# Kernel optimization log

Hardware: AMD Instinct MI355X
Metric: run time of the kernel (lower is better)

## Reference

```python
import jax, jax.numpy as jnp
import numpy as np

B, N, M, D = 32, 500, 500, 256
SQRT_D = 16.0
LOGIT_CLIP = 10.0


def setup_inputs() -> dict:
    key = jax.random.key(0)
    ks = jax.random.split(key, 12)
    s = 1.0 / np.sqrt(D)
    return {
        "encoded_q0": jax.random.normal(ks[0], (B, N, D), jnp.float32),
        "encoded_jobs": jax.random.normal(ks[1], (B, M, D), jnp.float32),
        "encoded_q1": jax.random.normal(ks[2], (B, N, D), jnp.float32),
        "cur_cost_mat": jax.random.uniform(ks[3], (B, N, M), jnp.float32),
        "log_scale": jnp.ones((1,), jnp.float32),
        "ninf_mask": jnp.zeros((B, N, M), jnp.float32),
        "Wq0": jax.random.normal(ks[4], (D, D), jnp.float32) * s,
        "Wq1": jax.random.normal(ks[5], (D, D), jnp.float32) * s,
        "Wk": jax.random.normal(ks[6], (D, D), jnp.float32) * s,
        "Wv": jax.random.normal(ks[7], (D, D), jnp.float32) * s,
        "alpha1": jnp.ones((1,), jnp.float32),
        "alpha2": jnp.ones((1,), jnp.float32),
    }


def reference(encoded_q0, encoded_jobs, encoded_q1, cur_cost_mat, log_scale,
              ninf_mask, Wq0, Wq1, Wk, Wv, alpha1, alpha2):
    # precomputed state (set_kv / set_q1): Linear without bias -> x @ W.T
    k = jnp.einsum('bmd,ed->bme', encoded_jobs, Wk)
    v = jnp.einsum('bmd,ed->bme', encoded_jobs, Wv)
    q1 = jnp.einsum('bnd,ed->bne', encoded_q1, Wq1)
    q0 = jnp.einsum('bnd,ed->bne', encoded_q0, Wq0)
    q = q1 + q0

    # AAFM: adaptation bias = -alpha1 * log_scale * cost (+ ninf_mask)
    exp_bias = jnp.exp(-alpha1 * log_scale * cur_cost_mat + ninf_mask)  # (B,N,M)
    exp_k = jnp.exp(k)                                                   # (B,M,D)
    num = jnp.einsum('bnm,bmd->bnd', exp_bias, exp_k * v)
    den = jnp.einsum('bnm,bmd->bnd', exp_bias, exp_k)
    weighted = jnp.nan_to_num(num / den)
    aafm_out = jax.nn.sigmoid(q) * weighted                              # (B,N,D)

    # single-head scoring against raw encoded_jobs
    score = jnp.einsum('bnd,bmd->bnm', aafm_out, encoded_jobs)
    score = score / SQRT_D - alpha2 * log_scale * cur_cost_mat
    score = LOGIT_CLIP * jnp.tanh(score) + ninf_mask
    return jax.nn.softmax(score, axis=-1)
```

## Files before the change

### kernel.cpp

```cpp
#include <hip/hip_runtime.h>
#include <math.h>

using u16 = unsigned short;
typedef __attribute__((ext_vector_type(8))) short short8;
typedef __attribute__((ext_vector_type(16))) float floatx16;

constexpr int Bc = 32, Nn = 500, Mm = 500, Dd = 256;
constexpr float LOGIT_CLIP = 10.0f;
constexpr float INV_SQRT_D = 1.0f / 16.0f;

__device__ __forceinline__ floatx16 mfma32(short8 a, short8 b, floatx16 c) {
    return __builtin_amdgcn_mfma_f32_32x32x16_bf16(a, b, c, 0, 0, 0);
}

__device__ __forceinline__ floatx16 zero16() {
    floatx16 v = {0.f,0.f,0.f,0.f,0.f,0.f,0.f,0.f,0.f,0.f,0.f,0.f,0.f,0.f,0.f,0.f};
    return v;
}

__device__ __forceinline__ void gl_lds16(const u16* g, u16* l) {
    __builtin_amdgcn_global_load_lds(
        (const __attribute__((address_space(1))) unsigned int*)g,
        (__attribute__((address_space(3))) unsigned int*)l, 16, 0, 0);
}

__device__ __forceinline__ void split1(float x, u16& h, u16& l) {
    unsigned u = __float_as_uint(x);
    unsigned rh = (u + 0x7FFFu + ((u >> 16) & 1u)) & 0xFFFF0000u;
    float fh = __uint_as_float(rh);
    float fl = x - fh;
    unsigned ul = __float_as_uint(fl);
    unsigned rl = ul + 0x7FFFu + ((ul >> 16) & 1u);
    h = (u16)(rh >> 16);
    l = (u16)(rl >> 16);
}

__device__ __forceinline__ u16 bf16rtn(float x) {
    unsigned u = __float_as_uint(x);
    return (u16)((u + 0x7FFFu + ((u >> 16) & 1u)) >> 16);
}

__device__ __forceinline__ float fast_tanh(float x) {
    return 1.0f - 2.0f / (__expf(2.0f * x) + 1.0f);
}

__device__ __forceinline__ void split8(const float4& a, const float4& c,
                                       short8& hv, short8& lv) {
    u16 hh, ll;
    split1(a.x, hh, ll); hv[0] = (short)hh; lv[0] = (short)ll;
    split1(a.y, hh, ll); hv[1] = (short)hh; lv[1] = (short)ll;
    split1(a.z, hh, ll); hv[2] = (short)hh; lv[2] = (short)ll;
    split1(a.w, hh, ll); hv[3] = (short)hh; lv[3] = (short)ll;
    split1(c.x, hh, ll); hv[4] = (short)hh; lv[4] = (short)ll;
    split1(c.y, hh, ll); hv[5] = (short)hh; lv[5] = (short)ll;
    split1(c.z, hh, ll); hv[6] = (short)hh; lv[6] = (short)ll;
    split1(c.w, hh, ll); hv[7] = (short)hh; lv[7] = (short)ll;
}


__global__ __launch_bounds__(256) void k0w_pk(const float* __restrict__ s0,
                                              const float* __restrict__ s1,
                                              const float* __restrict__ s2,
                                              const float* __restrict__ s3,
                                              u16* __restrict__ pkw) {
    const float* s = blockIdx.y == 0 ? s0 : blockIdx.y == 1 ? s1 :
                     blockIdx.y == 2 ? s2 : s3;
    const int w = blockIdx.y;
    const int flat = (blockIdx.x * 256 + threadIdx.x) * 8;
    const int i = flat >> 8, j0 = flat & 255;
    float4 a = *(const float4*)&s[flat];
    float4 c = *(const float4*)&s[flat + 4];
    short8 hv, lv;
    split8(a, c, hv, lv);
    const int dt = i >> 5, i31 = i & 31, dc = j0 >> 4, hp = (j0 >> 3) & 1;
    const size_t off = (size_t)(w * 8 + dt) * 16384 + (size_t)dc * 1024
                     + (size_t)((hp << 5) | i31) * 8;
    *(short8*)&pkw[off] = hv;
    *(short8*)&pkw[off + 512] = lv;
}

__global__ __launch_bounds__(256) void k0pk3(const float* __restrict__ s0,
                                             const float* __restrict__ s1,
                                             const float* __restrict__ s2,
                                             u16* __restrict__ d0,
                                             u16* __restrict__ d1,
                                             u16* __restrict__ d2) {
    const float* s = blockIdx.y == 0 ? s0 : blockIdx.y == 1 ? s1 : s2;
    u16* d = blockIdx.y == 0 ? d0 : blockIdx.y == 1 ? d1 : d2;
    const int bx = blockIdx.x;
    const int b = bx >> 6;
    const int chunk = bx & 63;
    const int flat = threadIdx.x * 8;
    const int lr = flat >> 8;
    const int j0 = flat & 255;
    const int pr = chunk * 8 + lr;
    short8 hv = {0,0,0,0,0,0,0,0}, lv = {0,0,0,0,0,0,0,0};
    if (pr < Nn) {
        const size_t o = ((size_t)b * Nn + pr) * Dd + j0;
        float4 a = *(const float4*)&s[o];
        float4 c = *(const float4*)&s[o + 4];
        split8(a, c, hv, lv);
    }
    const int mt = pr >> 5, r31 = pr & 31;
    const int dc = j0 >> 4, hp = (j0 >> 3) & 1;
    const size_t off = (size_t)(b * 16 + mt) * 16384 + (size_t)dc * 1024
                     + (size_t)((hp << 5) | r31) * 8;
    *(short8*)&d[off] = hv;
    *(short8*)&d[off + 512] = lv;
}

__global__ __launch_bounds__(256) void kexp_pk(const float* __restrict__ cost,
                                               const float* __restrict__ mask,
                                               const float* __restrict__ alpha1,
                                               const float* __restrict__ lsc,
                                               u16* __restrict__ pka) {
    __shared__ u16 tile[32][520];
    const float a1ls = alpha1[0] * lsc[0];
    const int b = blockIdx.x >> 4, nt = blockIdx.x & 15;
    const int t = threadIdx.x;
#pragma unroll
    for (int q = 0; q < 8; ++q) {
        const int flat = (q << 11) + (t << 3);
        const int nl = flat >> 9, m = flat & 511;
        const int n = min(nt * 32 + nl, Nn - 1);
        const size_t o = ((size_t)b * Nn + n) * Mm + m;
        ushort4 w0 = {0, 0, 0, 0}, w1 = {0, 0, 0, 0};
        if (m <= 488) {
            float4 c0 = *(const float4*)&cost[o];
            float4 c1 = *(const float4*)&cost[o + 4];
            float4 k0 = *(const float4*)&mask[o];
            float4 k1 = *(const float4*)&mask[o + 4];
            w0.x = bf16rtn(__expf(fmaf(-a1ls, c0.x, k0.x)));
            w0.y = bf16rtn(__expf(fmaf(-a1ls, c0.y, k0.y)));
            w0.z = bf16rtn(__expf(fmaf(-a1ls, c0.z, k0.z)));
            w0.w = bf16rtn(__expf(fmaf(-a1ls, c0.w, k0.w)));
            w1.x = bf16rtn(__expf(fmaf(-a1ls, c1.x, k1.x)));
            w1.y = bf16rtn(__expf(fmaf(-a1ls, c1.y, k1.y)));
            w1.z = bf16rtn(__expf(fmaf(-a1ls, c1.z, k1.z)));
            w1.w = bf16rtn(__expf(fmaf(-a1ls, c1.w, k1.w)));
        } else if (m == 496) {
            float4 c0 = *(const float4*)&cost[o];
            float4 k0 = *(const float4*)&mask[o];
            w0.x = bf16rtn(__expf(fmaf(-a1ls, c0.x, k0.x)));
            w0.y = bf16rtn(__expf(fmaf(-a1ls, c0.y, k0.y)));
            w0.z = bf16rtn(__expf(fmaf(-a1ls, c0.z, k0.z)));
            w0.w = bf16rtn(__expf(fmaf(-a1ls, c0.w, k0.w)));
        }
        *(ushort4*)&tile[nl][m] = w0;
        *(ushort4*)&tile[nl][m + 4] = w1;
    }
    __syncthreads();
    const int lane = t & 63, wvv = t >> 6;
    const int n31 = lane & 31, hh = lane >> 5;
    const size_t pbase = (size_t)(b * 16 + nt) * 16384 + (size_t)lane * 8;
#pragma unroll
    for (int q = 0; q < 8; ++q) {
        const int mc = wvv * 8 + q;
        short8 v = *(const short8*)&tile[n31][mc * 16 + hh * 8];
        *(short8*)&pka[pbase + (size_t)mc * 512] = v;
    }
}

__global__ __launch_bounds__(256) void k1_kv(const u16* __restrict__ pkj,
                                             const u16* __restrict__ pkw,
                                             u16* __restrict__ pkb) {
    const int lane = threadIdx.x & 63, wv = threadIdx.x >> 6;
    const int l31 = lane & 31, h = lane >> 5;
    const int b = blockIdx.z;
    const int dt = blockIdx.y * 4 + wv;
    const int mt = blockIdx.x;
    const int M0 = mt * 32;

    const size_t wk  = (size_t)dt * 16384 + (size_t)lane * 8;
    const size_t wvb = (size_t)(8 + dt) * 16384 + (size_t)lane * 8;
    const size_t jb  = (size_t)(b * 16 + mt) * 16384 + (size_t)lane * 8;

    floatx16 ak = zero16(), av = zero16();

    short8 buf[3][6];
#define K1L(S, DC) { \
    buf[S][0] = *(const short8*)(pkw + wk  + (size_t)(DC) * 1024); \
    buf[S][1] = *(const short8*)(pkw + wk  + (size_t)(DC) * 1024 + 512); \
    buf[S][2] = *(const short8*)(pkw + wvb + (size_t)(DC) * 1024); \
    buf[S][3] = *(const short8*)(pkw + wvb + (size_t)(DC) * 1024 + 512); \
    buf[S][4] = *(const short8*)(pkj + jb  + (size_t)(DC) * 1024); \
    buf[S][5] = *(const short8*)(pkj + jb  + (size_t)(DC) * 1024 + 512); }

    K1L(0, 0)
    K1L(1, 1)
#pragma unroll
    for (int it = 0; it < 16; ++it) {
        if (it + 2 < 16) { K1L((it + 2) % 3, it + 2) }
        const int c = it % 3;
        ak = mfma32(buf[c][0], buf[c][4], ak);
        ak = mfma32(buf[c][0], buf[c][5], ak);
        ak = mfma32(buf[c][1], buf[c][4], ak);
        av = mfma32(buf[c][2], buf[c][4], av);
        av = mfma32(buf[c][2], buf[c][5], av);
        av = mfma32(buf[c][3], buf[c][4], av);
    }
#undef K1L

    const int hp = (l31 >> 3) & 1, ee = l31 & 7, mcl = l31 >> 4;
    const size_t sb0 = ((size_t)b * 8 + dt) * 65536
                     + (size_t)(mt * 2 + mcl) * 2048 + (size_t)hp * 256 + ee;
    const bool v0 = (M0 + l31) < Mm;
#pragma unroll
    for (int r = 0; r < 16; ++r) {
        const int d31 = (r & 3) + ((r >> 2) << 3) + (h << 2);
        const size_t o = sb0 + (size_t)d31 * 8;
        u16 hh, ll;
        const float ek = v0 ? __expf(ak[r]) : 0.f;
        const float ev = v0 ? ek * av[r] : 0.f;
        split1(ek, hh, ll); pkb[o] = hh; pkb[o + 512] = ll;
        split1(ev, hh, ll); pkb[o + 1024] = hh; pkb[o + 1536] = ll;
    }
}

__global__ __launch_bounds__(256) void k2_q(const u16* __restrict__ pkq0,
                                            const u16* __restrict__ pkq1,
                                            const u16* __restrict__ pkw,
                                            float* __restrict__ sq) {
    const int lane = threadIdx.x & 63, wv = threadIdx.x >> 6;
    const int l31 = lane & 31, h = lane >> 5;
    const int b = blockIdx.y;
    const int nt = blockIdx.x;
    const int N0 = nt * 32;
    const int dt0 = wv;
    const int dt1 = wv + 4;

    const size_t qa  = (size_t)(b * 16 + nt) * 16384 + (size_t)lane * 8;
    const size_t w00 = (size_t)(16 + dt0) * 16384 + (size_t)lane * 8;
    const size_t w10 = (size_t)(24 + dt0) * 16384 + (size_t)lane * 8;
    const size_t w01 = (size_t)(16 + dt1) * 16384 + (size_t)lane * 8;
    const size_t w11 = (size_t)(24 + dt1) * 16384 + (size_t)lane * 8;

    floatx16 acc0 = zero16(), acc1 = zero16();

    short8 buf[3][12];
#define K2L(S, DC) { \
    buf[S][0]  = *(const short8*)(pkq0 + qa + (size_t)(DC) * 1024); \
    buf[S][1]  = *(const short8*)(pkq0 + qa + (size_t)(DC) * 1024 + 512); \
    buf[S][2]  = *(const short8*)(pkq1 + qa + (size_t)(DC) * 1024); \
    buf[S][3]  = *(const short8*)(pkq1 + qa + (size_t)(DC) * 1024 + 512); \
    buf[S][4]  = *(const short8*)(pkw + w00 + (size_t)(DC) * 1024); \
    buf[S][5]  = *(const short8*)(pkw + w00 + (size_t)(DC) * 1024 + 512); \
    buf[S][6]  = *(const short8*)(pkw + w10 + (size_t)(DC) * 1024); \
    buf[S][7]  = *(const short8*)(pkw + w10 + (size_t)(DC) * 1024 + 512); \
    buf[S][8]  = *(const short8*)(pkw + w01 + (size_t)(DC) * 1024); \
    buf[S][9]  = *(const short8*)(pkw + w01 + (size_t)(DC) * 1024 + 512); \
    buf[S][10] = *(const short8*)(pkw + w11 + (size_t)(DC) * 1024); \
    buf[S][11] = *(const short8*)(pkw + w11 + (size_t)(DC) * 1024 + 512); }

    K2L(0, 0)
    K2L(1, 1)
#pragma unroll
    for (int it = 0; it < 16; ++it) {
        if (it + 2 < 16) { K2L((it + 2) % 3, it + 2) }
        const int c = it % 3;
        acc0 = mfma32(buf[c][0], buf[c][4], acc0);
        acc0 = mfma32(buf[c][0], buf[c][5], acc0);
        acc0 = mfma32(buf[c][1], buf[c][4], acc0);
        acc0 = mfma32(buf[c][2], buf[c][6], acc0);
        acc0 = mfma32(buf[c][2], buf[c][7], acc0);
        acc0 = mfma32(buf[c][3], buf[c][6], acc0);
        acc1 = mfma32(buf[c][0], buf[c][8], acc1);
        acc1 = mfma32(buf[c][0], buf[c][9], acc1);
        acc1 = mfma32(buf[c][1], buf[c][8], acc1);
        acc1 = mfma32(buf[c][2], buf[c][10], acc1);
        acc1 = mfma32(buf[c][2], buf[c][11], acc1);
        acc1 = mfma32(buf[c][3], buf[c][10], acc1);
    }
#undef K2L

#pragma unroll
    for (int r = 0; r < 16; ++r) {
        const int n = N0 + (r & 3) + ((r >> 2) << 3) + (h << 2);
        if (n < Nn) {
            const size_t o = ((size_t)b * Nn + n) * Dd + l31;
            sq[o + dt0 * 32] = 1.0f / (1.0f + __expf(-acc0[r]));
            sq[o + dt1 * 32] = 1.0f / (1.0f + __expf(-acc1[r]));
        }
    }
}

__global__ __launch_bounds__(256) void k3_aafm(const u16* __restrict__ pka,
                                               const u16* __restrict__ pkb,
                                               const float* __restrict__ sq,
                                               u16* __restrict__ pkc) {
    __shared__ u16 bbuf[2][8192];
    const int i = blockIdx.x;
    const int x = i & 7, j = i >> 3;
    const int nt = j & 15;
    const int dh = (j >> 4) & 1;
    const int b = ((j >> 5) << 3) + x;
    const int t = threadIdx.x;
    const int lane = t & 63, wv = t >> 6;
    const int l31 = lane & 31, h = lane >> 5;
    const int N0 = nt << 5;
    const int dt = dh * 4 + wv;

    const u16* pbB = pkb + ((size_t)b * 8 + dh * 4) * 65536;
    const size_t abase = (size_t)(b * 16 + nt) * 16384 + (size_t)lane * 8;

    floatx16 dn = zero16(), nm = zero16();

#define STG3(BUF, MC) { \
    { const int f = 0 * 2048 + t * 8; \
      gl_lds16(pbB + (size_t)(f >> 11) * 65536 + (size_t)(MC) * 2048 + (f & 2047), \
               &bbuf[BUF][0 * 2048 + wv * 512]); } \
    { const int f = 1 * 2048 + t * 8; \
      gl_lds16(pbB + (size_t)(f >> 11) * 65536 + (size_t)(MC) * 2048 + (f & 2047), \
               &bbuf[BUF][1 * 2048 + wv * 512]); } \
    { const int f = 2 * 2048 + t * 8; \
      gl_lds16(pbB + (size_t)(f >> 11) * 65536 + (size_t)(MC) * 2048 + (f & 2047), \
               &bbuf[BUF][2 * 2048 + wv * 512]); } \
    { const int f = 3 * 2048 + t * 8; \
      gl_lds16(pbB + (size_t)(f >> 11) * 65536 + (size_t)(MC) * 2048 + (f & 2047), \
               &bbuf[BUF][3 * 2048 + wv * 512]); } }

    STG3(0, 0)
    short8 aa[2];
    aa[0] = *(const short8*)(pka + abase);
    __syncthreads();
#pragma unroll
    for (int mc = 0; mc < 32; ++mc) {
        const int cur = mc & 1, nxt = cur ^ 1;
        if (mc + 1 < 32) {
            STG3(nxt, mc + 1)
            aa[nxt] = *(const short8*)(pka + abase + (size_t)(mc + 1) * 512);
        }
        const u16* bp = &bbuf[cur][wv * 2048];
        short8 ekh = *(const short8*)(bp + (size_t)lane * 8);
        short8 ekl = *(const short8*)(bp + 512 + (size_t)lane * 8);
        short8 evh = *(const short8*)(bp + 1024 + (size_t)lane * 8);
        short8 evl = *(const short8*)(bp + 1536 + (size_t)lane * 8);
        dn = mfma32(aa[cur], ekh, dn);
        dn = mfma32(aa[cur], ekl, dn);
        nm = mfma32(aa[cur], evh, nm);
        nm = mfma32(aa[cur], evl, nm);
        __syncthreads();
    }
#undef STG3

    const int hp = (l31 >> 3) & 1, ee = l31 & 7;
    const int dcol = dt * 32 + l31;
    const int dc0 = dcol >> 4;
    const size_t cb0 = (size_t)(b * 16 + nt) * 16384 + (size_t)dc0 * 1024
                     + (size_t)hp * 256 + ee;
#pragma unroll
    for (int r = 0; r < 16; ++r) {
        const int n31 = (r & 3) + ((r >> 2) << 3) + (h << 2);
        const int n = N0 + n31;
        if (n < Nn) {
            const size_t so = ((size_t)b * Nn + n) * Dd + dcol;
            const size_t o = cb0 + (size_t)n31 * 8;
            u16 hh, ll;
            const float d0 = dn[r];
            const float w0 = (d0 != 0.f) ? nm[r] / d0 : 0.f;
            split1(sq[so] * w0, hh, ll);
            pkc[o] = hh; pkc[o + 512] = ll;
        }
    }
}

__global__ __launch_bounds__(512) void k4_score(const u16* __restrict__ pkc,
                                                const u16* __restrict__ pkj,
                                                const float* __restrict__ cost,
                                                const float* __restrict__ mask,
                                                const float* __restrict__ alpha2,
                                                const float* __restrict__ lsc,
                                                float* __restrict__ out) {
    __shared__ u16 bb[2][16384];
    float (*pred)[8] = (float(*)[8])bb;
    const int i = blockIdx.x;
    const int x = i & 7, j = i >> 3;
    const int nt = j & 15;
    const int b = ((j >> 4) << 3) + x;
    const int t = threadIdx.x;
    const int lane = t & 63, wv = t >> 6;
    const int l31 = lane & 31, h = lane >> 5;
    const int N0 = nt << 5;
    const float a2ls = alpha2[0] * lsc[0];

    const u16* jbB = pkj + (size_t)b * 16 * 16384;
    const size_t ab = (size_t)(b * 16 + nt) * 16384 + (size_t)lane * 8;
    const int m0g = wv * 64 + l31;
    const int m1g = m0g + 32;

    floatx16 acc0 = zero16(), acc1 = zero16();

#define STG4(BUF, DC) { \
    { const int f = 0 * 4096 + t * 8; \
      gl_lds16(jbB + (size_t)(f >> 10) * 16384 + (size_t)(DC) * 1024 + (f & 1023), \
               &bb[BUF][0 * 4096 + wv * 512]); } \
    { const int f = 1 * 4096 + t * 8; \
      gl_lds16(jbB + (size_t)(f >> 10) * 16384 + (size_t)(DC) * 1024 + (f & 1023), \
               &bb[BUF][1 * 4096 + wv * 512]); } \
    { const int f = 2 * 4096 + t * 8; \
      gl_lds16(jbB + (size_t)(f >> 10) * 16384 + (size_t)(DC) * 1024 + (f & 1023), \
               &bb[BUF][2 * 4096 + wv * 512]); } \
    { const int f = 3 * 4096 + t * 8; \
      gl_lds16(jbB + (size_t)(f >> 10) * 16384 + (size_t)(DC) * 1024 + (f & 1023), \
               &bb[BUF][3 * 4096 + wv * 512]); } }

    STG4(0, 0)
    short8 aH[2], aL[2];
    aH[0] = *(const short8*)(pkc + ab);
    aL[0] = *(const short8*)(pkc + ab + 512);
    __syncthreads();
#pragma unroll
    for (int dc = 0; dc < 16; ++dc) {
        const int cur = dc & 1, nxt = cur ^ 1;
        if (dc + 1 < 16) {
            STG4(nxt, dc + 1)
            aH[nxt] = *(const short8*)(pkc + ab + (size_t)(dc + 1) * 1024);
            aL[nxt] = *(const short8*)(pkc + ab + (size_t)(dc + 1) * 1024 + 512);
        }
        const u16* bp = &bb[cur][wv * 2048];
        short8 b0h = *(const short8*)(bp + (size_t)lane * 8);
        short8 b0l = *(const short8*)(bp + 512 + (size_t)lane * 8);
        short8 b1h = *(const short8*)(bp + 1024 + (size_t)lane * 8);
        short8 b1l = *(const short8*)(bp + 1536 + (size_t)lane * 8);
        acc0 = mfma32(aH[cur], b0h, acc0);
        acc0 = mfma32(aH[cur], b0l, acc0);
        acc0 = mfma32(aL[cur], b0h, acc0);
        acc1 = mfma32(aH[cur], b1h, acc1);
        acc1 = mfma32(aH[cur], b1l, acc1);
        acc1 = mfma32(aL[cur], b1h, acc1);
        __syncthreads();
    }
#undef STG4

    float lg0[16], lg1[16];
    const size_t cb = (size_t)b * Nn * Mm;
#pragma unroll
    for (int r = 0; r < 16; ++r) {
        const int row = (r & 3) + ((r >> 2) << 3) + (h << 2);
        const int n = N0 + row;
        if (n < Nn) {
            const size_t o = cb + (size_t)n * Mm + m0g;
            lg0[r] = LOGIT_CLIP * fast_tanh(fmaf(-a2ls, cost[o], acc0[r] * INV_SQRT_D)) + mask[o];
            if (m1g < Mm) {
                const size_t o1 = o + 32;
                lg1[r] = LOGIT_CLIP * fast_tanh(fmaf(-a2ls, cost[o1], acc1[r] * INV_SQRT_D)) + mask[o1];
            } else lg1[r] = -1e30f;
        } else { lg0[r] = -1e30f; lg1[r] = -1e30f; }
    }

    float rm[16];
#pragma unroll
    for (int r = 0; r < 16; ++r) rm[r] = fmaxf(lg0[r], lg1[r]);
#pragma unroll
    for (int d = 1; d < 32; d <<= 1)
#pragma unroll
        for (int r = 0; r < 16; ++r) rm[r] = fmaxf(rm[r], __shfl_xor(rm[r], d));
    if (l31 == 0) {
#pragma unroll
        for (int r = 0; r < 16; ++r)
            pred[(r & 3) + ((r >> 2) << 3) + (h << 2)][wv] = rm[r];
    }
    __syncthreads();
    float fm[16];
#pragma unroll
    for (int r = 0; r < 16; ++r) {
        const int row = (r & 3) + ((r >> 2) << 3) + (h << 2);
        float v = pred[row][0];
#pragma unroll
        for (int w = 1; w < 8; ++w) v = fmaxf(v, pred[row][w]);
        fm[r] = v;
    }
    __syncthreads();

    float sm[16];
#pragma unroll
    for (int r = 0; r < 16; ++r) {
        lg0[r] = __expf(lg0[r] - fm[r]);
        lg1[r] = __expf(lg1[r] - fm[r]);
        sm[r] = lg0[r] + lg1[r];
    }
#pragma unroll
    for (int d = 1; d < 32; d <<= 1)
#pragma unroll
        for (int r = 0; r < 16; ++r) sm[r] += __shfl_xor(sm[r], d);
    if (l31 == 0) {
#pragma unroll
        for (int r = 0; r < 16; ++r)
            pred[(r & 3) + ((r >> 2) << 3) + (h << 2)][wv] = sm[r];
    }
    __syncthreads();

#pragma unroll
    for (int r = 0; r < 16; ++r) {
        const int row = (r & 3) + ((r >> 2) << 3) + (h << 2);
        const int n = N0 + row;
        if (n < Nn) {
            float s = pred[row][0];
#pragma unroll
            for (int w = 1; w < 8; ++w) s += pred[row][w];
            const float inv = 1.0f / s;
            const size_t o = cb + (size_t)n * Mm + m0g;
            out[o] = lg0[r] * inv;
            if (m1g < Mm) out[o + 32] = lg1[r] * inv;
        }
    }
}

extern "C" void kernel_launch(void* const* d_in, const int* in_sizes, int n_in,
                              void* d_out, int out_size, void* d_ws, size_t ws_size,
                              hipStream_t stream) {
    const float* q0        = (const float*)d_in[0];
    const float* jobs      = (const float*)d_in[1];
    const float* q1        = (const float*)d_in[2];
    const float* cost      = (const float*)d_in[3];
    const float* log_scale = (const float*)d_in[4];
    const float* mask      = (const float*)d_in[5];
    const float* Wq0       = (const float*)d_in[6];
    const float* Wq1       = (const float*)d_in[7];
    const float* Wk        = (const float*)d_in[8];
    const float* Wv        = (const float*)d_in[9];
    const float* alpha1    = (const float*)d_in[10];
    const float* alpha2    = (const float*)d_in[11];
    float* out = (float*)d_out;

    const size_t PK_SZ  = (size_t)Bc * 16 * 16384;
    const size_t PKW_SZ = (size_t)4 * 8 * 16384;
    const size_t PKB_SZ = (size_t)Bc * 8 * 65536;

    u16* ws   = (u16*)d_ws;
    u16* pkj  = ws;
    u16* pkq0 = ws + PK_SZ;
    u16* pkq1 = ws + 2 * PK_SZ;
    u16* pkw  = ws + 3 * PK_SZ;
    u16* pkb  = pkw + PKW_SZ;
    float* sq = (float*)(pkb + PKB_SZ);

    u16* pka = pkq1;
    u16* pkc = pkq0;
    (void)ws_size;

    dim3 blk(256);
    k0w_pk<<<dim3(32, 4), blk, 0, stream>>>(Wk, Wv, Wq0, Wq1, pkw);
    k0pk3<<<dim3(2048, 3), blk, 0, stream>>>(jobs, q0, q1, pkj, pkq0, pkq1);
    k1_kv<<<dim3(16, 2, 32), blk, 0, stream>>>(pkj, pkw, pkb);
    k2_q<<<dim3(16, 32), blk, 0, stream>>>(pkq0, pkq1, pkw, sq);
    kexp_pk<<<512, blk, 0, stream>>>(cost, mask, alpha1, log_scale, pka);
    k3_aafm<<<1024, blk, 0, stream>>>(pka, pkb, sq, pkc);
    k4_score<<<512, dim3(512), 0, stream>>>(pkc, pkj, cost, mask,
                                            alpha2, log_scale, out);
}
```

Measured before the change: 302.2 us.

## Fuse q packing into k2_q and exp-bias packing into k3_aafm

```diff
diff --git a/kernel.cpp b/kernel.cpp
--- a/kernel.cpp
+++ b/kernel.cpp
@@ -79,14 +79,8 @@
     *(short8*)&pkw[off + 512] = lv;
 }
 
-__global__ __launch_bounds__(256) void k0pk3(const float* __restrict__ s0,
-                                             const float* __restrict__ s1,
-                                             const float* __restrict__ s2,
-                                             u16* __restrict__ d0,
-                                             u16* __restrict__ d1,
-                                             u16* __restrict__ d2) {
-    const float* s = blockIdx.y == 0 ? s0 : blockIdx.y == 1 ? s1 : s2;
-    u16* d = blockIdx.y == 0 ? d0 : blockIdx.y == 1 ? d1 : d2;
+__global__ __launch_bounds__(256) void k0pkj(const float* __restrict__ s,
+                                             u16* __restrict__ d) {
     const int bx = blockIdx.x;
     const int b = bx >> 6;
     const int chunk = bx & 63;
@@ -109,20 +103,191 @@
     *(short8*)&d[off + 512] = lv;
 }
 
-__global__ __launch_bounds__(256) void kexp_pk(const float* __restrict__ cost,
+__global__ __launch_bounds__(256) void k1_kv(const u16* __restrict__ pkj,
+                                             const u16* __restrict__ pkw,
+                                             u16* __restrict__ pkb) {
+    const int lane = threadIdx.x & 63, wv = threadIdx.x >> 6;
+    const int l31 = lane & 31, h = lane >> 5;
+    const int b = blockIdx.z;
+    const int dt = blockIdx.y * 4 + wv;
+    const int mt = blockIdx.x;
+    const int M0 = mt * 32;
+
+    const size_t wk  = (size_t)dt * 16384 + (size_t)lane * 8;
+    const size_t wvb = (size_t)(8 + dt) * 16384 + (size_t)lane * 8;
+    const size_t jb  = (size_t)(b * 16 + mt) * 16384 + (size_t)lane * 8;
+
+    floatx16 ak = zero16(), av = zero16();
+
+    short8 buf[3][6];
+#define K1L(S, DC) { \
+    buf[S][0] = *(const short8*)(pkw + wk  + (size_t)(DC) * 1024); \
+    buf[S][1] = *(const short8*)(pkw + wk  + (size_t)(DC) * 1024 + 512); \
+    buf[S][2] = *(const short8*)(pkw + wvb + (size_t)(DC) * 1024); \
+    buf[S][3] = *(const short8*)(pkw + wvb + (size_t)(DC) * 1024 + 512); \
+    buf[S][4] = *(const short8*)(pkj + jb  + (size_t)(DC) * 1024); \
+    buf[S][5] = *(const short8*)(pkj + jb  + (size_t)(DC) * 1024 + 512); }
+
+    K1L(0, 0)
+    K1L(1, 1)
+#pragma unroll
+    for (int it = 0; it < 16; ++it) {
+        if (it + 2 < 16) { K1L((it + 2) % 3, it + 2) }
+        const int c = it % 3;
+        ak = mfma32(buf[c][0], buf[c][4], ak);
+        ak = mfma32(buf[c][0], buf[c][5], ak);
+        ak = mfma32(buf[c][1], buf[c][4], ak);
+        av = mfma32(buf[c][2], buf[c][4], av);
+        av = mfma32(buf[c][2], buf[c][5], av);
+        av = mfma32(buf[c][3], buf[c][4], av);
+    }
+#undef K1L
+
+    const int hp = (l31 >> 3) & 1, ee = l31 & 7, mcl = l31 >> 4;
+    const size_t sb0 = ((size_t)b * 8 + dt) * 65536
+                     + (size_t)(mt * 2 + mcl) * 2048 + (size_t)hp * 256 + ee;
+    const bool v0 = (M0 + l31) < Mm;
+#pragma unroll
+    for (int r = 0; r < 16; ++r) {
+        const int d31 = (r & 3) + ((r >> 2) << 3) + (h << 2);
+        const size_t o = sb0 + (size_t)d31 * 8;
+        u16 hh, ll;
+        const float ek = v0 ? __expf(ak[r]) : 0.f;
+        const float ev = v0 ? ek * av[r] : 0.f;
+        split1(ek, hh, ll); pkb[o] = hh; pkb[o + 512] = ll;
+        split1(ev, hh, ll); pkb[o + 1024] = hh; pkb[o + 1536] = ll;
+    }
+}
+
+__global__ __launch_bounds__(256) void k2_q(const float* __restrict__ q0,
+                                            const float* __restrict__ q1,
+                                            const u16* __restrict__ pkw,
+                                            float* __restrict__ sq) {
+    __shared__ u16 tq[4][32][264];
+    const int t = threadIdx.x;
+    const int lane = t & 63, wv = t >> 6;
+    const int l31 = lane & 31, h = lane >> 5;
+    const int b = blockIdx.y;
+    const int nt = blockIdx.x;
+
+#pragma unroll
+    for (int s = 0; s < 2; ++s) {
+        const float* src = s ? q1 : q0;
+#pragma unroll
+        for (int it = 0; it < 4; ++it) {
+            const int flat = (it * 256 + t) * 8;
+            const int nl = flat >> 8, j0 = flat & 255;
+            const int n = min(nt * 32 + nl, Nn - 1);
+            const size_t o = ((size_t)b * Nn + n) * Dd + j0;
+            float4 a = *(const float4*)&src[o];
+            float4 c = *(const float4*)&src[o + 4];
+            short8 hv, lv;
+            split8(a, c, hv, lv);
+            *(short8*)&tq[s * 2][nl][j0] = hv;
+            *(short8*)&tq[s * 2 + 1][nl][j0] = lv;
+        }
+    }
+    __syncthreads();
+
+    const int dt0 = wv;
+    const int dt1 = wv + 4;
+    const size_t w00 = (size_t)(16 + dt0) * 16384 + (size_t)lane * 8;
+    const size_t w10 = (size_t)(24 + dt0) * 16384 + (size_t)lane * 8;
+    const size_t w01 = (size_t)(16 + dt1) * 16384 + (size_t)lane * 8;
+    const size_t w11 = (size_t)(24 + dt1) * 16384 + (size_t)lane * 8;
+
+    floatx16 acc0 = zero16(), acc1 = zero16();
+
+    short8 buf[3][8];
+#define K2L(S, DC) { \
+    buf[S][0] = *(const short8*)(pkw + w00 + (size_t)(DC) * 1024); \
+    buf[S][1] = *(const short8*)(pkw + w00 + (size_t)(DC) * 1024 + 512); \
+    buf[S][2] = *(const short8*)(pkw + w10 + (size_t)(DC) * 1024); \
+    buf[S][3] = *(const short8*)(pkw + w10 + (size_t)(DC) * 1024 + 512); \
+    buf[S][4] = *(const short8*)(pkw + w01 + (size_t)(DC) * 1024); \
+    buf[S][5] = *(const short8*)(pkw + w01 + (size_t)(DC) * 1024 + 512); \
+    buf[S][6] = *(const short8*)(pkw + w11 + (size_t)(DC) * 1024); \
+    buf[S][7] = *(const short8*)(pkw + w11 + (size_t)(DC) * 1024 + 512); }
+
+    K2L(0, 0)
+    K2L(1, 1)
+#pragma unroll
+    for (int it = 0; it < 16; ++it) {
+        if (it + 2 < 16) { K2L((it + 2) % 3, it + 2) }
+        const int c = it % 3;
+        const int co = it * 16 + h * 8;
+        short8 a0h = *(const short8*)&tq[0][l31][co];
+        short8 a0l = *(const short8*)&tq[1][l31][co];
+        short8 a1h = *(const short8*)&tq[2][l31][co];
+        short8 a1l = *(const short8*)&tq[3][l31][co];
+        acc0 = mfma32(a0h, buf[c][0], acc0);
+        acc0 = mfma32(a0h, buf[c][1], acc0);
+        acc0 = mfma32(a0l, buf[c][0], acc0);
+        acc0 = mfma32(a1h, buf[c][2], acc0);
+        acc0 = mfma32(a1h, buf[c][3], acc0);
+        acc0 = mfma32(a1l, buf[c][2], acc0);
+        acc1 = mfma32(a0h, buf[c][4], acc1);
+        acc1 = mfma32(a0h, buf[c][5], acc1);
+        acc1 = mfma32(a0l, buf[c][4], acc1);
+        acc1 = mfma32(a1h, buf[c][6], acc1);
+        acc1 = mfma32(a1h, buf[c][7], acc1);
+        acc1 = mfma32(a1l, buf[c][6], acc1);
+    }
+#undef K2L
+
+    float* sp0 = sq + ((((size_t)b * 16 + nt) * 8 + dt0) * 64 + lane) * 16;
+    float* sp1 = sq + ((((size_t)b * 16 + nt) * 8 + dt1) * 64 + lane) * 16;
+#pragma unroll
+    for (int r = 0; r < 16; ++r) {
+        sp0[r] = 1.0f / (1.0f + __expf(-acc0[r]));
+        sp1[r] = 1.0f / (1.0f + __expf(-acc1[r]));
+    }
+}
+
+__global__ __launch_bounds__(256) void k3_aafm(const float* __restrict__ cost,
                                                const float* __restrict__ mask,
                                                const float* __restrict__ alpha1,
                                                const float* __restrict__ lsc,
-                                               u16* __restrict__ pka) {
+                                               const u16* __restrict__ pkb,
+                                               const float* __restrict__ sq,
+                                               u16* __restrict__ pkc) {
     __shared__ u16 tile[32][520];
+    __shared__ u16 bbuf[2][8192];
+    const int i = blockIdx.x;
+    const int x = i & 7, j = i >> 3;
+    const int nt = j & 15;
+    const int dh = (j >> 4) & 1;
+    const int b = ((j >> 5) << 3) + x;
+    const int t = threadIdx.x;
+    const int lane = t & 63, wv = t >> 6;
+    const int l31 = lane & 31, h = lane >> 5;
+    const int N0 = nt << 5;
+    const int dt = dh * 4 + wv;
+
+    const u16* pbB = pkb + ((size_t)b * 8 + dh * 4) * 65536;
+
+#define STG3(BUF, MC) { \
+    { const int f = 0 * 2048 + t * 8; \
+      gl_lds16(pbB + (size_t)(f >> 11) * 65536 + (size_t)(MC) * 2048 + (f & 2047), \
+               &bbuf[BUF][0 * 2048 + wv * 512]); } \
+    { const int f = 1 * 2048 + t * 8; \
+      gl_lds16(pbB + (size_t)(f >> 11) * 65536 + (size_t)(MC) * 2048 + (f & 2047), \
+               &bbuf[BUF][1 * 2048 + wv * 512]); } \
+    { const int f = 2 * 2048 + t * 8; \
+      gl_lds16(pbB + (size_t)(f >> 11) * 65536 + (size_t)(MC) * 2048 + (f & 2047), \
+               &bbuf[BUF][2 * 2048 + wv * 512]); } \
+    { const int f = 3 * 2048 + t * 8; \
+      gl_lds16(pbB + (size_t)(f >> 11) * 65536 + (size_t)(MC) * 2048 + (f & 2047), \
+               &bbuf[BUF][3 * 2048 + wv * 512]); } }
+
+    STG3(0, 0)
+
     const float a1ls = alpha1[0] * lsc[0];
-    const int b = blockIdx.x >> 4, nt = blockIdx.x & 15;
-    const int t = threadIdx.x;
 #pragma unroll
     for (int q = 0; q < 8; ++q) {
         const int flat = (q << 11) + (t << 3);
         const int nl = flat >> 9, m = flat & 511;
-        const int n = min(nt * 32 + nl, Nn - 1);
+        const int n = min(N0 + nl, Nn - 1);
         const size_t o = ((size_t)b * Nn + n) * Mm + m;
         ushort4 w0 = {0, 0, 0, 0}, w1 = {0, 0, 0, 0};
         if (m <= 488) {
@@ -150,199 +315,27 @@
         *(ushort4*)&tile[nl][m + 4] = w1;
     }
     __syncthreads();
-    const int lane = t & 63, wvv = t >> 6;
-    const int n31 = lane & 31, hh = lane >> 5;
-    const size_t pbase = (size_t)(b * 16 + nt) * 16384 + (size_t)lane * 8;
-#pragma unroll
-    for (int q = 0; q < 8; ++q) {
-        const int mc = wvv * 8 + q;
-        short8 v = *(const short8*)&tile[n31][mc * 16 + hh * 8];
-        *(short8*)&pka[pbase + (size_t)mc * 512] = v;
-    }
-}
-
-__global__ __launch_bounds__(256) void k1_kv(const u16* __restrict__ pkj,
-                                             const u16* __restrict__ pkw,
-                                             u16* __restrict__ pkb) {
-    const int lane = threadIdx.x & 63, wv = threadIdx.x >> 6;
-    const int l31 = lane & 31, h = lane >> 5;
-    const int b = blockIdx.z;
-    const int dt = blockIdx.y * 4 + wv;
-    const int mt = blockIdx.x;
-    const int M0 = mt * 32;
-
-    const size_t wk  = (size_t)dt * 16384 + (size_t)lane * 8;
-    const size_t wvb = (size_t)(8 + dt) * 16384 + (size_t)lane * 8;
-    const size_t jb  = (size_t)(b * 16 + mt) * 16384 + (size_t)lane * 8;
-
-    floatx16 ak = zero16(), av = zero16();
-
-    short8 buf[3][6];
-#define K1L(S, DC) { \
-    buf[S][0] = *(const short8*)(pkw + wk  + (size_t)(DC) * 1024); \
-    buf[S][1] = *(const short8*)(pkw + wk  + (size_t)(DC) * 1024 + 512); \
-    buf[S][2] = *(const short8*)(pkw + wvb + (size_t)(DC) * 1024); \
-    buf[S][3] = *(const short8*)(pkw + wvb + (size_t)(DC) * 1024 + 512); \
-    buf[S][4] = *(const short8*)(pkj + jb  + (size_t)(DC) * 1024); \
-    buf[S][5] = *(const short8*)(pkj + jb  + (size_t)(DC) * 1024 + 512); }
-
-    K1L(0, 0)
-    K1L(1, 1)
-#pragma unroll
-    for (int it = 0; it < 16; ++it) {
-        if (it + 2 < 16) { K1L((it + 2) % 3, it + 2) }
-        const int c = it % 3;
-        ak = mfma32(buf[c][0], buf[c][4], ak);
-        ak = mfma32(buf[c][0], buf[c][5], ak);
-        ak = mfma32(buf[c][1], buf[c][4], ak);
-        av = mfma32(buf[c][2], buf[c][4], av);
-        av = mfma32(buf[c][2], buf[c][5], av);
-        av = mfma32(buf[c][3], buf[c][4], av);
-    }
-#undef K1L
-
-    const int hp = (l31 >> 3) & 1, ee = l31 & 7, mcl = l31 >> 4;
-    const size_t sb0 = ((size_t)b * 8 + dt) * 65536
-                     + (size_t)(mt * 2 + mcl) * 2048 + (size_t)hp * 256 + ee;
-    const bool v0 = (M0 + l31) < Mm;
-#pragma unroll
-    for (int r = 0; r < 16; ++r) {
-        const int d31 = (r & 3) + ((r >> 2) << 3) + (h << 2);
-        const size_t o = sb0 + (size_t)d31 * 8;
-        u16 hh, ll;
-        const float ek = v0 ? __expf(ak[r]) : 0.f;
-        const float ev = v0 ? ek * av[r] : 0.f;
-        split1(ek, hh, ll); pkb[o] = hh; pkb[o + 512] = ll;
-        split1(ev, hh, ll); pkb[o + 1024] = hh; pkb[o + 1536] = ll;
-    }
-}
-
-__global__ __launch_bounds__(256) void k2_q(const u16* __restrict__ pkq0,
-                                            const u16* __restrict__ pkq1,
-                                            const u16* __restrict__ pkw,
-                                            float* __restrict__ sq) {
-    const int lane = threadIdx.x & 63, wv = threadIdx.x >> 6;
-    const int l31 = lane & 31, h = lane >> 5;
-    const int b = blockIdx.y;
-    const int nt = blockIdx.x;
-    const int N0 = nt * 32;
-    const int dt0 = wv;
-    const int dt1 = wv + 4;
-
-    const size_t qa  = (size_t)(b * 16 + nt) * 16384 + (size_t)lane * 8;
-    const size_t w00 = (size_t)(16 + dt0) * 16384 + (size_t)lane * 8;
-    const size_t w10 = (size_t)(24 + dt0) * 16384 + (size_t)lane * 8;
-    const size_t w01 = (size_t)(16 + dt1) * 16384 + (size_t)lane * 8;
-    const size_t w11 = (size_t)(24 + dt1) * 16384 + (size_t)lane * 8;
-
-    floatx16 acc0 = zero16(), acc1 = zero16();
-
-    short8 buf[3][12];
-#define K2L(S, DC) { \
-    buf[S][0]  = *(const short8*)(pkq0 + qa + (size_t)(DC) * 1024); \
-    buf[S][1]  = *(const short8*)(pkq0 + qa + (size_t)(DC) * 1024 + 512); \
-    buf[S][2]  = *(const short8*)(pkq1 + qa + (size_t)(DC) * 1024); \
-    buf[S][3]  = *(const short8*)(pkq1 + qa + (size_t)(DC) * 1024 + 512); \
-    buf[S][4]  = *(const short8*)(pkw + w00 + (size_t)(DC) * 1024); \
-    buf[S][5]  = *(const short8*)(pkw + w00 + (size_t)(DC) * 1024 + 512); \
-    buf[S][6]  = *(const short8*)(pkw + w10 + (size_t)(DC) * 1024); \
-    buf[S][7]  = *(const short8*)(pkw + w10 + (size_t)(DC) * 1024 + 512); \
-    buf[S][8]  = *(const short8*)(pkw + w01 + (size_t)(DC) * 1024); \
-    buf[S][9]  = *(const short8*)(pkw + w01 + (size_t)(DC) * 1024 + 512); \
-    buf[S][10] = *(const short8*)(pkw + w11 + (size_t)(DC) * 1024); \
-    buf[S][11] = *(const short8*)(pkw + w11 + (size_t)(DC) * 1024 + 512); }
-
-    K2L(0, 0)
-    K2L(1, 1)
-#pragma unroll
-    for (int it = 0; it < 16; ++it) {
-        if (it + 2 < 16) { K2L((it + 2) % 3, it + 2) }
-        const int c = it % 3;
-        acc0 = mfma32(buf[c][0], buf[c][4], acc0);
-        acc0 = mfma32(buf[c][0], buf[c][5], acc0);
-        acc0 = mfma32(buf[c][1], buf[c][4], acc0);
-        acc0 = mfma32(buf[c][2], buf[c][6], acc0);
-        acc0 = mfma32(buf[c][2], buf[c][7], acc0);
-        acc0 = mfma32(buf[c][3], buf[c][6], acc0);
-        acc1 = mfma32(buf[c][0], buf[c][8], acc1);
-        acc1 = mfma32(buf[c][0], buf[c][9], acc1);
-        acc1 = mfma32(buf[c][1], buf[c][8], acc1);
-        acc1 = mfma32(buf[c][2], buf[c][10], acc1);
-        acc1 = mfma32(buf[c][2], buf[c][11], acc1);
-        acc1 = mfma32(buf[c][3], buf[c][10], acc1);
-    }
-#undef K2L
-
-#pragma unroll
-    for (int r = 0; r < 16; ++r) {
-        const int n = N0 + (r & 3) + ((r >> 2) << 3) + (h << 2);
-        if (n < Nn) {
-            const size_t o = ((size_t)b * Nn + n) * Dd + l31;
-            sq[o + dt0 * 32] = 1.0f / (1.0f + __expf(-acc0[r]));
-            sq[o + dt1 * 32] = 1.0f / (1.0f + __expf(-acc1[r]));
-        }
-    }
-}
-
-__global__ __launch_bounds__(256) void k3_aafm(const u16* __restrict__ pka,
-                                               const u16* __restrict__ pkb,
-                                               const float* __restrict__ sq,
-                                               u16* __restrict__ pkc) {
-    __shared__ u16 bbuf[2][8192];
-    const int i = blockIdx.x;
-    const int x = i & 7, j = i >> 3;
-    const int nt = j & 15;
-    const int dh = (j >> 4) & 1;
-    const int b = ((j >> 5) << 3) + x;
-    const int t = threadIdx.x;
-    const int lane = t & 63, wv = t >> 6;
-    const int l31 = lane & 31, h = lane >> 5;
-    const int N0 = nt << 5;
-    const int dt = dh * 4 + wv;
-
-    const u16* pbB = pkb + ((size_t)b * 8 + dh * 4) * 65536;
-    const size_t abase = (size_t)(b * 16 + nt) * 16384 + (size_t)lane * 8;
 
     floatx16 dn = zero16(), nm = zero16();
-
-#define STG3(BUF, MC) { \
-    { const int f = 0 * 2048 + t * 8; \
-      gl_lds16(pbB + (size_t)(f >> 11) * 65536 + (size_t)(MC) * 2048 + (f & 2047), \
-               &bbuf[BUF][0 * 2048 + wv * 512]); } \
-    { const int f = 1 * 2048 + t * 8; \
-      gl_lds16(pbB + (size_t)(f >> 11) * 65536 + (size_t)(MC) * 2048 + (f & 2047), \
-               &bbuf[BUF][1 * 2048 + wv * 512]); } \
-    { const int f = 2 * 2048 + t * 8; \
-      gl_lds16(pbB + (size_t)(f >> 11) * 65536 + (size_t)(MC) * 2048 + (f & 2047), \
-               &bbuf[BUF][2 * 2048 + wv * 512]); } \
-    { const int f = 3 * 2048 + t * 8; \
-      gl_lds16(pbB + (size_t)(f >> 11) * 65536 + (size_t)(MC) * 2048 + (f & 2047), \
-               &bbuf[BUF][3 * 2048 + wv * 512]); } }
-
-    STG3(0, 0)
-    short8 aa[2];
-    aa[0] = *(const short8*)(pka + abase);
-    __syncthreads();
 #pragma unroll
     for (int mc = 0; mc < 32; ++mc) {
         const int cur = mc & 1, nxt = cur ^ 1;
-        if (mc + 1 < 32) {
-            STG3(nxt, mc + 1)
-            aa[nxt] = *(const short8*)(pka + abase + (size_t)(mc + 1) * 512);
-        }
+        if (mc + 1 < 32) { STG3(nxt, mc + 1) }
+        short8 aa = *(const short8*)&tile[l31][mc * 16 + h * 8];
         const u16* bp = &bbuf[cur][wv * 2048];
         short8 ekh = *(const short8*)(bp + (size_t)lane * 8);
         short8 ekl = *(const short8*)(bp + 512 + (size_t)lane * 8);
         short8 evh = *(const short8*)(bp + 1024 + (size_t)lane * 8);
         short8 evl = *(const short8*)(bp + 1536 + (size_t)lane * 8);
-        dn = mfma32(aa[cur], ekh, dn);
-        dn = mfma32(aa[cur], ekl, dn);
-        nm = mfma32(aa[cur], evh, nm);
-        nm = mfma32(aa[cur], evl, nm);
+        dn = mfma32(aa, ekh, dn);
+        dn = mfma32(aa, ekl, dn);
+        nm = mfma32(aa, evh, nm);
+        nm = mfma32(aa, evl, nm);
         __syncthreads();
     }
 #undef STG3
 
+    const float* sp = sq + ((((size_t)b * 16 + nt) * 8 + dt) * 64 + lane) * 16;
     const int hp = (l31 >> 3) & 1, ee = l31 & 7;
     const int dcol = dt * 32 + l31;
     const int dc0 = dcol >> 4;
@@ -353,12 +346,11 @@
         const int n31 = (r & 3) + ((r >> 2) << 3) + (h << 2);
         const int n = N0 + n31;
         if (n < Nn) {
-            const size_t so = ((size_t)b * Nn + n) * Dd + dcol;
             const size_t o = cb0 + (size_t)n31 * 8;
             u16 hh, ll;
             const float d0 = dn[r];
             const float w0 = (d0 != 0.f) ? nm[r] / d0 : 0.f;
-            split1(sq[so] * w0, hh, ll);
+            split1(sp[r] * w0, hh, ll);
             pkc[o] = hh; pkc[o + 512] = ll;
         }
     }
@@ -526,26 +518,22 @@
     const size_t PK_SZ  = (size_t)Bc * 16 * 16384;
     const size_t PKW_SZ = (size_t)4 * 8 * 16384;
     const size_t PKB_SZ = (size_t)Bc * 8 * 65536;
+    const size_t SQ_SZ  = (size_t)Bc * 16 * 8 * 64 * 16;
 
     u16* ws   = (u16*)d_ws;
     u16* pkj  = ws;
-    u16* pkq0 = ws + PK_SZ;
-    u16* pkq1 = ws + 2 * PK_SZ;
-    u16* pkw  = ws + 3 * PK_SZ;
+    u16* pkw  = ws + PK_SZ;
     u16* pkb  = pkw + PKW_SZ;
     float* sq = (float*)(pkb + PKB_SZ);
-
-    u16* pka = pkq1;
-    u16* pkc = pkq0;
+    u16* pkc  = (u16*)(sq + SQ_SZ);
     (void)ws_size;
 
     dim3 blk(256);
     k0w_pk<<<dim3(32, 4), blk, 0, stream>>>(Wk, Wv, Wq0, Wq1, pkw);
-    k0pk3<<<dim3(2048, 3), blk, 0, stream>>>(jobs, q0, q1, pkj, pkq0, pkq1);
+    k0pkj<<<2048, blk, 0, stream>>>(jobs, pkj);
     k1_kv<<<dim3(16, 2, 32), blk, 0, stream>>>(pkj, pkw, pkb);
-    k2_q<<<dim3(16, 32), blk, 0, stream>>>(pkq0, pkq1, pkw, sq);
-    kexp_pk<<<512, blk, 0, stream>>>(cost, mask, alpha1, log_scale, pka);
-    k3_aafm<<<1024, blk, 0, stream>>>(pka, pkb, sq, pkc);
+    k2_q<<<dim3(16, 32), blk, 0, stream>>>(q0, q1, pkw, sq);
+    k3_aafm<<<1024, blk, 0, stream>>>(cost, mask, alpha1, log_scale, pkb, sq, pkc);
     k4_score<<<512, dim3(512), 0, stream>>>(pkc, pkj, cost, mask,
                                             alpha2, log_scale, out);
 }
```

New measurement: 299.2 us. About the same (-1.0%).
